# Kernel optimization log

Measured on AMD Instinct MI355X. Metric: run time of the kernel, lower is better.

Reference implementation:

```python
import jax, jax.numpy as jnp
import numpy as np

NHEADS = 16
HEAD_DIM = 64
HIDDEN = 1024
QKV = NHEADS * HEAD_DIM  # 1024
SCALING = HEAD_DIM ** -0.5


def setup_inputs() -> dict:
    key = jax.random.key(0)
    k1, k2, k3, k4, k5 = jax.random.split(key, 5)
    B, S = 2, 2048
    hidden_states = jax.random.normal(k1, (B, S, HIDDEN), dtype=jnp.float32)
    # nn.Linear weights: stored [out, in]; kaiming-uniform-ish init scale
    w_qkv = jax.random.normal(k2, (3 * QKV, HIDDEN), dtype=jnp.float32) * (HIDDEN ** -0.5)
    b_qkv = jax.random.normal(k3, (3 * QKV,), dtype=jnp.float32) * 0.01
    w_o = jax.random.normal(k4, (HIDDEN, QKV), dtype=jnp.float32) * (QKV ** -0.5)
    b_o = jax.random.normal(k5, (HIDDEN,), dtype=jnp.float32) * 0.01
    return {"hidden_states": hidden_states, "w_qkv": w_qkv, "b_qkv": b_qkv,
            "w_o": w_o, "b_o": b_o}


def reference(hidden_states, w_qkv, b_qkv, w_o, b_o):
    B, S, _ = hidden_states.shape
    # qkv projection: x @ W^T + b  (torch nn.Linear convention)
    qkv = jnp.einsum('bsh,oh->bso', hidden_states, w_qkv) + b_qkv  # [B,S,3*QKV]
    xq, xk, xv = jnp.split(qkv, 3, axis=-1)
    # [B,S,H,D] -> [B,H,S,D]
    q = xq.reshape(B, S, NHEADS, HEAD_DIM).transpose(0, 2, 1, 3)
    k = xk.reshape(B, S, NHEADS, HEAD_DIM).transpose(0, 2, 1, 3)
    v = xv.reshape(B, S, NHEADS, HEAD_DIM).transpose(0, 2, 1, 3)
    scores = jnp.einsum('bhqd,bhkd->bhqk', q, k) * SCALING
    # dropout is identity in eval mode; mask is None in this config
    probs = jax.nn.softmax(scores.astype(jnp.float32), axis=-1).astype(q.dtype)
    out = jnp.einsum('bhqk,bhkd->bhqd', probs, v)  # [B,H,S,D]
    out = out.transpose(0, 2, 1, 3).reshape(B, S, QKV)
    return jnp.einsum('bsq,oq->bso', out, w_o) + b_o
```

## Files before the change

kernel.cpp:

```cpp
#include <hip/hip_runtime.h>

#define SEQ     2048
#define MROWS   4096
#define HID     1024
#define QKV3    3072
#define NH      16
#define HD      64
#define QSCALE  0.18033688f

typedef unsigned short u16;
typedef unsigned int   u32;
typedef __attribute__((ext_vector_type(8)))  short  bf16x8;
typedef __attribute__((ext_vector_type(4)))  float  floatx4;
typedef __attribute__((ext_vector_type(16))) float  floatx16;
typedef __attribute__((ext_vector_type(4)))  unsigned int u32x4;

__device__ __forceinline__ u16 f2bf(float f) {
    u32 u = __builtin_bit_cast(u32, f);
    u += 0x7fffu + ((u >> 16) & 1u);
    return (u16)(u >> 16);
}

#if __has_builtin(__builtin_amdgcn_exp2f)
__device__ __forceinline__ float fast_exp2(float x) { return __builtin_amdgcn_exp2f(x); }
#else
__device__ __forceinline__ float fast_exp2(float x) { return exp2f(x); }
#endif

#if __has_builtin(__builtin_amdgcn_cvt_pk_bf16_f32)
__device__ __forceinline__ u32 pack_bf(float a, float b) {
    auto r = __builtin_amdgcn_cvt_pk_bf16_f32(a, b);
    return __builtin_bit_cast(u32, r);
}
#else
__device__ __forceinline__ u32 pack_bf(float a, float b) {
    u32 ua = __builtin_bit_cast(u32, a) + 0x8000u;
    u32 ub = __builtin_bit_cast(u32, b) + 0x8000u;
    return __builtin_amdgcn_perm(ub, ua, 0x07060302u);
}
#endif

__device__ __forceinline__ void plane_swap(u32 &x, u32 &y) {
#if __has_builtin(__builtin_amdgcn_permlane32_swap)
    typedef __attribute__((ext_vector_type(2))) unsigned int u32x2;
    u32x2 r = __builtin_amdgcn_permlane32_swap(x, y, false, false);
    x = r[0]; y = r[1];
#else
    asm volatile("v_permlane32_swap_b32 %0, %1" : "+v"(x), "+v"(y));
#endif
}

__device__ __forceinline__ void async_cp16(const void* g, void* l) {
    __builtin_amdgcn_global_load_lds(
        (const __attribute__((address_space(1))) unsigned int*)g,
        (__attribute__((address_space(3))) unsigned int*)l, 16, 0, 0);
}

#define N4_X   (MROWS * HID / 4)
#define N4_WQ  (QKV3 * HID / 4)
#define N4_WO  (HID * HID / 4)
__global__ void cvt_all(const float* __restrict__ x, const float* __restrict__ wq,
                        const float* __restrict__ wo, u16* __restrict__ xb,
                        u16* __restrict__ wqb, u16* __restrict__ wob) {
    int i = blockIdx.x * blockDim.x + threadIdx.x;
    const float* src; u16* dst; int k;
    if (i < N4_X)                { src = x;  dst = xb;  k = i; }
    else if (i < N4_X + N4_WQ)   { src = wq; dst = wqb; k = i - N4_X; }
    else                         { src = wo; dst = wob; k = i - N4_X - N4_WQ; }
    float4 v = ((const float4*)src)[k];
    uint2 o = {pack_bf(v.x, v.y), pack_bf(v.z, v.w)};
    ((uint2*)dst)[k] = o;
}

template <int MODE, int NT>
__global__ __launch_bounds__(256)
void gemm_bf16_nt(const u16* __restrict__ A, const u16* __restrict__ B,
                  const float* __restrict__ bias, float* __restrict__ Cout,
                  int M, int N, int K,
                  u16* __restrict__ q_ws, u16* __restrict__ k_ws,
                  u16* __restrict__ vt_ws) {
    constexpr int WN = NT / 2;
    constexpr int NJ = WN / 32;
    __shared__ __align__(16) u16 smemS[3 * 128 * 32 + 3 * NT * 32];
    auto As_ = [&](int bb) -> u16* { return smemS + bb * 4096; };
    auto Bs_ = [&](int bb) -> u16* { return smemS + 12288 + bb * (NT * 32); };
    const int t  = (int)threadIdx.x;
    const int w  = t >> 6, l = t & 63;
    const int wr = w >> 1, wc = w & 1;
    const int m0 = (int)blockIdx.y * 128, n0 = (int)blockIdx.x * NT;
    const int lrow = l >> 2;
    const int lseg = ((l & 3) ^ ((l >> 3) & 3)) * 8;
    const int ql = l & 31, h = l >> 5;

    auto stage = [&](int k0, int bb) {
#pragma unroll
        for (int rep = 0; rep < 2; ++rep) {
            const int chunk = w + rep * 4;
            const int row   = chunk * 16 + lrow;
            async_cp16(A + (size_t)(m0 + row) * K + k0 + lseg, As_(bb) + chunk * 512);
            if (NT == 128 || rep == 0)
                async_cp16(B + (size_t)(n0 + row) * K + k0 + lseg, Bs_(bb) + chunk * 512);
        }
    };

    const floatx16 z16 = (floatx16)(0.f);
    floatx16 acc[2][NJ];
#pragma unroll
    for (int i = 0; i < 2; ++i)
#pragma unroll
        for (int j = 0; j < NJ; ++j) acc[i][j] = z16;

    const int T = K >> 5;
    stage(0, 0);
    stage(32, 1);
    for (int tt = 0; tt < T; ++tt) {
        const int cur = tt % 3;
        if (tt + 1 < T) {
            if constexpr (NT == 128) asm volatile("s_waitcnt vmcnt(4)" ::: "memory");
            else                     asm volatile("s_waitcnt vmcnt(3)" ::: "memory");
        } else {
            asm volatile("s_waitcnt vmcnt(0)" ::: "memory");
        }
        __builtin_amdgcn_s_barrier();
        bf16x8 af[2][2], bfr[NJ][2];
#pragma unroll
        for (int i = 0; i < 2; ++i)
#pragma unroll
            for (int ks = 0; ks < 2; ++ks) {
                const int row = wr * 64 + i * 32 + ql;
                const int seg = ((ks * 2 + h) ^ ((ql >> 1) & 3)) * 8;
                af[i][ks] = *(const bf16x8*)(As_(cur) + row * 32 + seg);
            }
#pragma unroll
        for (int j = 0; j < NJ; ++j)
#pragma unroll
            for (int ks = 0; ks < 2; ++ks) {
                const int row = wc * WN + j * 32 + ql;
                const int seg = ((ks * 2 + h) ^ ((ql >> 1) & 3)) * 8;
                bfr[j][ks] = *(const bf16x8*)(Bs_(cur) + row * 32 + seg);
            }
        if (tt + 2 < T) stage((tt + 2) << 5, (tt + 2) % 3);
#pragma unroll
        for (int i = 0; i < 2; ++i)
#pragma unroll
            for (int j = 0; j < NJ; ++j)
#pragma unroll
                for (int ks = 0; ks < 2; ++ks)
                    acc[i][j] = __builtin_amdgcn_mfma_f32_32x32x16_bf16(
                        af[i][ks], bfr[j][ks], acc[i][j], 0, 0, 0);
    }

    if (MODE == 1 && (n0 >> 10) == 2) {
        __syncthreads();
        u32* VT = (u32*)smemS;
#pragma unroll
        for (int j = 0; j < NJ; ++j) {
            const int lc = wc * WN + j * 32 + ql;
            const float bv = bias[n0 + lc];
#pragma unroll
            for (int i = 0; i < 2; ++i) {
#pragma unroll
                for (int g = 0; g < 4; ++g) {
                    const int rl0 = wr * 64 + i * 32 + g * 8 + h * 4;
                    const int wp = rl0 >> 1;
                    uint2 pr = {pack_bf(acc[i][j][4*g+0] + bv, acc[i][j][4*g+1] + bv),
                                pack_bf(acc[i][j][4*g+2] + bv, acc[i][j][4*g+3] + bv)};
                    *(uint2*)&VT[lc * 64 + (wp ^ ((lc & 7) << 3))] = pr;
                }
            }
        }
        __syncthreads();
        const int lc = t >> 1, h2 = t & 1;
        const int gcol = n0 + lc;
        const int hh = (gcol >> 6) & 15, d = gcol & 63;
        const int b = m0 >> 11;
        u16* __restrict__ dstp = vt_ws
            + ((size_t)(b * NH + hh) * HD + d) * SEQ + (m0 & 2047) + h2 * 64;
        const int X = (lc & 7) << 3;
#pragma unroll
        for (int c = 0; c < 8; ++c) {
            u32x4 v = *(const u32x4*)&VT[lc * 64 + ((h2 * 32 + c * 4) ^ X)];
            *(u32x4*)&dstp[c * 8] = v;
        }
        return;
    }

#pragma unroll
    for (int j = 0; j < NJ; ++j) {
        const int col = n0 + wc * WN + j * 32 + ql;
        const float bv = bias[col];
        const int region = col >> 10;
        const int hh = (col >> 6) & 15, d = col & 63;
#pragma unroll
        for (int i = 0; i < 2; ++i) {
#pragma unroll
            for (int g = 0; g < 4; ++g) {
                const int row0 = m0 + wr * 64 + i * 32 + g * 8 + h * 4;
                if (MODE == 0) {
#pragma unroll
                    for (int r = 0; r < 4; ++r)
                        Cout[(size_t)(row0 + r) * N + col] = acc[i][j][4*g+r] + bv;
                } else {
                    u16* __restrict__ dst = (region == 0) ? q_ws : k_ws;
                    const float sc = (region == 0) ? QSCALE : 1.0f;
#pragma unroll
                    for (int r = 0; r < 4; ++r) {
                        const int row = row0 + r;
                        const int b = row >> 11, s = row & 2047;
                        dst[((size_t)(b * NH + hh) * SEQ + s) * HD + d] =
                            f2bf((acc[i][j][4*g+r] + bv) * sc);
                    }
                }
            }
        }
    }
}

__global__ __launch_bounds__(256, 2)
void attn_mfma(const u16* __restrict__ qw, const u16* __restrict__ kw,
               const u16* __restrict__ vtw, u16* __restrict__ attn) {
    __shared__ u16 Ks [2][2][64 * 64];
    __shared__ u16 Vts[2][2][64 * 64];

    const int bh   = (int)blockIdx.x;
    const int qblk = (int)blockIdx.y * 128;
    const int t = (int)threadIdx.x;
    const int w = t >> 6, l = t & 63;
    const int ql = l & 31, h = l >> 5;
    const int srow = l >> 3, sseg = l & 7;
    const size_t headSD = (size_t)bh * SEQ * HD;
    const size_t headDS = (size_t)bh * HD * SEQ;

    auto stage = [&](int it, int bb) {
#pragma unroll
        for (int half = 0; half < 2; ++half) {
            const int kt = it * 2 + half;
#pragma unroll
            for (int rep = 0; rep < 2; ++rep) {
                const int chunk = w * 2 + rep;
                async_cp16(kw + headSD + (size_t)(kt * 64 + chunk * 8 + srow) * HD
                               + ((sseg ^ srow) * 8), &Ks[bb][half][chunk * 512]);
                async_cp16(vtw + headDS + (size_t)(chunk * 8 + srow) * SEQ + kt * 64
                               + ((sseg ^ srow) * 8), &Vts[bb][half][chunk * 512]);
            }
        }
    };

    bf16x8 qa[4];
#pragma unroll
    for (int ks = 0; ks < 4; ++ks)
        qa[ks] = *(const bf16x8*)(qw + headSD
            + (size_t)(qblk + w * 32 + ql) * HD + ks * 16 + h * 8);

    const floatx16 z16 = (floatx16)(0.f);
    floatx16 oacc[2];
    oacc[0] = z16; oacc[1] = z16;
    float2 psum2 = {0.f, 0.f};

    stage(0, 0);
    for (int it = 0; it < SEQ / 128; ++it) {
        const int cur = it & 1;
        __syncthreads();
        if (it + 1 < SEQ / 128) stage(it + 1, cur ^ 1);

        floatx16 sacc[2][2];
#pragma unroll
        for (int half = 0; half < 2; ++half) {
#pragma unroll
            for (int ks = 0; ks < 4; ++ks) {
                const int seg = ((ks * 2 + h) ^ (ql & 7)) * 8;
#pragma unroll
                for (int t2 = 0; t2 < 2; ++t2) {
                    bf16x8 ka = *(const bf16x8*)&Ks[cur][half][(t2 * 32 + ql) * 64 + seg];
                    sacc[half][t2] = __builtin_amdgcn_mfma_f32_32x32x16_bf16(
                        ka, qa[ks], (ks == 0) ? z16 : sacc[half][t2], 0, 0, 0);
                }
            }
        }

#pragma unroll
        for (int half = 0; half < 2; ++half) {
#pragma unroll
            for (int t2 = 0; t2 < 2; ++t2) {
                u32 aw[8];
#pragma unroll
                for (int i = 0; i < 8; ++i) {
                    const float p0 = fast_exp2(sacc[half][t2][2 * i]);
                    const float p1 = fast_exp2(sacc[half][t2][2 * i + 1]);
                    psum2 += float2{p0, p1};
                    aw[i] = pack_bf(p0, p1);
                }
                plane_swap(aw[0], aw[2]); plane_swap(aw[1], aw[3]);
                plane_swap(aw[4], aw[6]); plane_swap(aw[5], aw[7]);

#pragma unroll
                for (int ks2 = 0; ks2 < 2; ++ks2) {
                    u32x4 pw = {aw[4 * ks2 + 0], aw[4 * ks2 + 1],
                                aw[4 * ks2 + 2], aw[4 * ks2 + 3]};
                    bf16x8 pb = __builtin_bit_cast(bf16x8, pw);
                    const int seg = ((t2 * 4 + ks2 * 2 + h) ^ (ql & 7)) * 8;
#pragma unroll
                    for (int dt = 0; dt < 2; ++dt) {
                        bf16x8 va = *(const bf16x8*)&Vts[cur][half][(dt * 32 + ql) * 64 + seg];
                        oacc[dt] = __builtin_amdgcn_mfma_f32_32x32x16_bf16(
                            va, pb, oacc[dt], 0, 0, 0);
                    }
                }
            }
        }
    }

    float psum = psum2.x + psum2.y;
    psum += __shfl_xor(psum, 32);
    const float inv = 1.0f / psum;

    const int b = bh >> 4, head = bh & 15;
    u16* __restrict__ orow =
        attn + (size_t)(b * SEQ + qblk + w * 32 + ql) * HID + head * HD;
#pragma unroll
    for (int dt = 0; dt < 2; ++dt) {
#pragma unroll
        for (int g = 0; g < 4; ++g) {
            uint2 o = {pack_bf(oacc[dt][g * 4 + 0] * inv, oacc[dt][g * 4 + 1] * inv),
                       pack_bf(oacc[dt][g * 4 + 2] * inv, oacc[dt][g * 4 + 3] * inv)};
            *(uint2*)&orow[dt * 32 + g * 8 + h * 4] = o;
        }
    }
}

extern "C" void kernel_launch(void* const* d_in, const int* in_sizes, int n_in,
                              void* d_out, int out_size, void* d_ws, size_t ws_size,
                              hipStream_t stream) {
    const float* x     = (const float*)d_in[0];
    const float* w_qkv = (const float*)d_in[1];
    const float* b_qkv = (const float*)d_in[2];
    const float* w_o   = (const float*)d_in[3];
    const float* b_o   = (const float*)d_in[4];
    float* outp = (float*)d_out;

    u16* xb    = (u16*)d_ws;
    u16* wqkvb = xb    + (size_t)MROWS * HID;
    u16* wob   = wqkvb + (size_t)QKV3 * HID;
    u16* q_ws  = wob   + (size_t)HID * HID;
    u16* k_ws  = q_ws  + (size_t)MROWS * HID;
    u16* vt_ws = k_ws  + (size_t)MROWS * HID;
    u16* attnb = vt_ws + (size_t)MROWS * HID;

    const int blk = 256;
    cvt_all<<<(N4_X + N4_WQ + N4_WO) / blk, blk, 0, stream>>>(
        x, w_qkv, w_o, xb, wqkvb, wob);

    gemm_bf16_nt<1, 128><<<dim3(QKV3 / 128, MROWS / 128), blk, 0, stream>>>(
        xb, wqkvb, b_qkv, nullptr, MROWS, QKV3, HID, q_ws, k_ws, vt_ws);

    attn_mfma<<<dim3(NH * 2, SEQ / 128), 256, 0, stream>>>(q_ws, k_ws, vt_ws, attnb);

    gemm_bf16_nt<0, 64><<<dim3(HID / 64, MROWS / 128), blk, 0, stream>>>(
        attnb, wob, b_o, outp, MROWS, HID, HID, nullptr, nullptr, nullptr);
}
```

Measured before the change: 183.4 us.

## Process two query tiles per wave in attention and widen output GEMM tile

```diff
diff --git a/kernel.cpp b/kernel.cpp
--- a/kernel.cpp
+++ b/kernel.cpp
@@ -216,14 +216,14 @@
     }
 }
 
-__global__ __launch_bounds__(256, 2)
+__global__ __launch_bounds__(256, 1)
 void attn_mfma(const u16* __restrict__ qw, const u16* __restrict__ kw,
                const u16* __restrict__ vtw, u16* __restrict__ attn) {
     __shared__ u16 Ks [2][2][64 * 64];
     __shared__ u16 Vts[2][2][64 * 64];
 
     const int bh   = (int)blockIdx.x;
-    const int qblk = (int)blockIdx.y * 128;
+    const int qblk = (int)blockIdx.y * 256;
     const int t = (int)threadIdx.x;
     const int w = t >> 6, l = t & 63;
     const int ql = l & 31, h = l >> 5;
@@ -246,16 +246,18 @@
         }
     };
 
-    bf16x8 qa[4];
-#pragma unroll
-    for (int ks = 0; ks < 4; ++ks)
-        qa[ks] = *(const bf16x8*)(qw + headSD
-            + (size_t)(qblk + w * 32 + ql) * HD + ks * 16 + h * 8);
+    bf16x8 qa[2][4];
+#pragma unroll
+    for (int qt = 0; qt < 2; ++qt)
+#pragma unroll
+        for (int ks = 0; ks < 4; ++ks)
+            qa[qt][ks] = *(const bf16x8*)(qw + headSD
+                + (size_t)(qblk + w * 64 + qt * 32 + ql) * HD + ks * 16 + h * 8);
 
     const floatx16 z16 = (floatx16)(0.f);
-    floatx16 oacc[2];
-    oacc[0] = z16; oacc[1] = z16;
-    float2 psum2 = {0.f, 0.f};
+    floatx16 oacc[2][2];
+    oacc[0][0] = z16; oacc[0][1] = z16; oacc[1][0] = z16; oacc[1][1] = z16;
+    float2 ps2[2] = {{0.f, 0.f}, {0.f, 0.f}};
 
     stage(0, 0);
     for (int it = 0; it < SEQ / 128; ++it) {
@@ -263,67 +265,74 @@
         __syncthreads();
         if (it + 1 < SEQ / 128) stage(it + 1, cur ^ 1);
 
-        floatx16 sacc[2][2];
 #pragma unroll
         for (int half = 0; half < 2; ++half) {
+            floatx16 sacc[2][2];
 #pragma unroll
             for (int ks = 0; ks < 4; ++ks) {
                 const int seg = ((ks * 2 + h) ^ (ql & 7)) * 8;
 #pragma unroll
                 for (int t2 = 0; t2 < 2; ++t2) {
                     bf16x8 ka = *(const bf16x8*)&Ks[cur][half][(t2 * 32 + ql) * 64 + seg];
-                    sacc[half][t2] = __builtin_amdgcn_mfma_f32_32x32x16_bf16(
-                        ka, qa[ks], (ks == 0) ? z16 : sacc[half][t2], 0, 0, 0);
-                }
-            }
-        }
-
-#pragma unroll
-        for (int half = 0; half < 2; ++half) {
+                    sacc[0][t2] = __builtin_amdgcn_mfma_f32_32x32x16_bf16(
+                        ka, qa[0][ks], (ks == 0) ? z16 : sacc[0][t2], 0, 0, 0);
+                    sacc[1][t2] = __builtin_amdgcn_mfma_f32_32x32x16_bf16(
+                        ka, qa[1][ks], (ks == 0) ? z16 : sacc[1][t2], 0, 0, 0);
+                }
+            }
+
 #pragma unroll
             for (int t2 = 0; t2 < 2; ++t2) {
-                u32 aw[8];
-#pragma unroll
-                for (int i = 0; i < 8; ++i) {
-                    const float p0 = fast_exp2(sacc[half][t2][2 * i]);
-                    const float p1 = fast_exp2(sacc[half][t2][2 * i + 1]);
-                    psum2 += float2{p0, p1};
-                    aw[i] = pack_bf(p0, p1);
-                }
-                plane_swap(aw[0], aw[2]); plane_swap(aw[1], aw[3]);
-                plane_swap(aw[4], aw[6]); plane_swap(aw[5], aw[7]);
+                u32 aw[2][8];
+#pragma unroll
+                for (int qt = 0; qt < 2; ++qt) {
+#pragma unroll
+                    for (int i = 0; i < 8; ++i) {
+                        const float p0 = fast_exp2(sacc[qt][t2][2 * i]);
+                        const float p1 = fast_exp2(sacc[qt][t2][2 * i + 1]);
+                        ps2[qt] += float2{p0, p1};
+                        aw[qt][i] = pack_bf(p0, p1);
+                    }
+                    plane_swap(aw[qt][0], aw[qt][2]); plane_swap(aw[qt][1], aw[qt][3]);
+                    plane_swap(aw[qt][4], aw[qt][6]); plane_swap(aw[qt][5], aw[qt][7]);
+                }
 
 #pragma unroll
                 for (int ks2 = 0; ks2 < 2; ++ks2) {
-                    u32x4 pw = {aw[4 * ks2 + 0], aw[4 * ks2 + 1],
-                                aw[4 * ks2 + 2], aw[4 * ks2 + 3]};
-                    bf16x8 pb = __builtin_bit_cast(bf16x8, pw);
                     const int seg = ((t2 * 4 + ks2 * 2 + h) ^ (ql & 7)) * 8;
+                    bf16x8 pb0 = __builtin_bit_cast(bf16x8,
+                        (u32x4){aw[0][4*ks2+0], aw[0][4*ks2+1], aw[0][4*ks2+2], aw[0][4*ks2+3]});
+                    bf16x8 pb1 = __builtin_bit_cast(bf16x8,
+                        (u32x4){aw[1][4*ks2+0], aw[1][4*ks2+1], aw[1][4*ks2+2], aw[1][4*ks2+3]});
 #pragma unroll
                     for (int dt = 0; dt < 2; ++dt) {
                         bf16x8 va = *(const bf16x8*)&Vts[cur][half][(dt * 32 + ql) * 64 + seg];
-                        oacc[dt] = __builtin_amdgcn_mfma_f32_32x32x16_bf16(
-                            va, pb, oacc[dt], 0, 0, 0);
+                        oacc[0][dt] = __builtin_amdgcn_mfma_f32_32x32x16_bf16(
+                            va, pb0, oacc[0][dt], 0, 0, 0);
+                        oacc[1][dt] = __builtin_amdgcn_mfma_f32_32x32x16_bf16(
+                            va, pb1, oacc[1][dt], 0, 0, 0);
                     }
                 }
             }
         }
     }
 
-    float psum = psum2.x + psum2.y;
-    psum += __shfl_xor(psum, 32);
-    const float inv = 1.0f / psum;
-
     const int b = bh >> 4, head = bh & 15;
-    u16* __restrict__ orow =
-        attn + (size_t)(b * SEQ + qblk + w * 32 + ql) * HID + head * HD;
-#pragma unroll
-    for (int dt = 0; dt < 2; ++dt) {
-#pragma unroll
-        for (int g = 0; g < 4; ++g) {
-            uint2 o = {pack_bf(oacc[dt][g * 4 + 0] * inv, oacc[dt][g * 4 + 1] * inv),
-                       pack_bf(oacc[dt][g * 4 + 2] * inv, oacc[dt][g * 4 + 3] * inv)};
-            *(uint2*)&orow[dt * 32 + g * 8 + h * 4] = o;
+#pragma unroll
+    for (int qt = 0; qt < 2; ++qt) {
+        float psum = ps2[qt].x + ps2[qt].y;
+        psum += __shfl_xor(psum, 32);
+        const float inv = 1.0f / psum;
+        u16* __restrict__ orow =
+            attn + (size_t)(b * SEQ + qblk + w * 64 + qt * 32 + ql) * HID + head * HD;
+#pragma unroll
+        for (int dt = 0; dt < 2; ++dt) {
+#pragma unroll
+            for (int g = 0; g < 4; ++g) {
+                uint2 o = {pack_bf(oacc[qt][dt][g * 4 + 0] * inv, oacc[qt][dt][g * 4 + 1] * inv),
+                           pack_bf(oacc[qt][dt][g * 4 + 2] * inv, oacc[qt][dt][g * 4 + 3] * inv)};
+                *(uint2*)&orow[dt * 32 + g * 8 + h * 4] = o;
+            }
         }
     }
 }
@@ -353,8 +362,8 @@
     gemm_bf16_nt<1, 128><<<dim3(QKV3 / 128, MROWS / 128), blk, 0, stream>>>(
         xb, wqkvb, b_qkv, nullptr, MROWS, QKV3, HID, q_ws, k_ws, vt_ws);
 
-    attn_mfma<<<dim3(NH * 2, SEQ / 128), 256, 0, stream>>>(q_ws, k_ws, vt_ws, attnb);
-
-    gemm_bf16_nt<0, 64><<<dim3(HID / 64, MROWS / 128), blk, 0, stream>>>(
+    attn_mfma<<<dim3(NH * 2, SEQ / 256), 256, 0, stream>>>(q_ws, k_ws, vt_ws, attnb);
+
+    gemm_bf16_nt<0, 128><<<dim3(HID / 128, MROWS / 128), blk, 0, stream>>>(
         attnb, wob, b_o, outp, MROWS, HID, HID, nullptr, nullptr, nullptr);
 }
```

Result: slower. 188.6 us (+2.8%).
